# Performance work log

Measured on AMD Instinct MI355X. Metric: run time of the kernel, lower is better.

Reference implementation:

```python
import jax, jax.numpy as jnp
import numpy as np

NUM_HEADS = 8
HEAD_DIM = 64  # hidden_dim // num_heads = 512 // 8
THRESHOLD = 0.5


def setup_inputs() -> dict:
    key = jax.random.key(0)
    ks = jax.random.split(key, 12)
    B, T, D, Hd = 4, 1024, 512, 512
    s = 0.02
    inp = {
        'x': jax.random.normal(ks[0], (B, T, D), dtype=jnp.float32),
        'Wq': jax.random.normal(ks[1], (D, Hd), dtype=jnp.float32) * s,
        'bq': jnp.zeros((Hd,), jnp.float32),
        'Wk': jax.random.normal(ks[2], (D, Hd), dtype=jnp.float32) * s,
        'bk': jnp.zeros((Hd,), jnp.float32),
        'Wv': jax.random.normal(ks[3], (D, Hd), dtype=jnp.float32) * s,
        'bv': jnp.zeros((Hd,), jnp.float32),
        'conv_w': jax.random.normal(ks[4], (NUM_HEADS,), dtype=jnp.float32) * 0.3,
        'conv_b': jnp.zeros((1,), jnp.float32),
        'Wfh': jax.random.normal(ks[5], (Hd, Hd), dtype=jnp.float32) * s,
        'bfh': jnp.zeros((Hd,), jnp.float32),
        'Wfg': jax.random.normal(ks[6], (Hd, Hd), dtype=jnp.float32) * s,
        'bfg': jnp.zeros((Hd,), jnp.float32),
        'Wrh': jax.random.normal(ks[7], (Hd, Hd), dtype=jnp.float32) * s,
        'brh': jnp.zeros((Hd,), jnp.float32),
        'Wrg': jax.random.normal(ks[8], (Hd, Hd), dtype=jnp.float32) * s,
        'brg': jnp.zeros((Hd,), jnp.float32),
    }
    return inp


def reference(x, Wq, bq, Wk, bk, Wv, bv, conv_w, conv_b,
              Wfh, bfh, Wfg, bfg, Wrh, brh, Wrg, brg):
    B, T, D = x.shape
    H, hd = NUM_HEADS, HEAD_DIM
    scale = hd ** -0.5

    q = (x @ Wq + bq).reshape(B, T, H, hd).transpose(0, 2, 1, 3)  # [B,H,T,hd]
    k = (x @ Wk + bk).reshape(B, T, H, hd).transpose(0, 2, 1, 3)
    v = (x @ Wv + bv).reshape(B, T, H, hd).transpose(0, 2, 1, 3)

    scores = jnp.einsum('bhqd,bhkd->bhqk', q, k) * scale        # [B,H,T,T]
    A_t = jax.nn.softmax(scores, axis=-1)

    # cross-head 1x1 conv: weighted sum over heads -> [B,1,T,T]
    R_f = jax.nn.sigmoid(jnp.einsum('bhqk,h->bqk', A_t, conv_w) + conv_b[0])
    R_f = R_f[:, None]                                           # [B,1,T,T]
    M_f = (R_f <= THRESHOLD).astype(A_t.dtype)
    M_r = (1.0 - R_f <= THRESHOLD).astype(A_t.dtype)

    A_f = jax.nn.softmax(A_t * M_f, axis=-1)
    A_r = jax.nn.softmax(A_t * M_r, axis=-1)

    T_f = jnp.einsum('bhqk,bhkd->bhqd', A_f, v).transpose(0, 2, 1, 3).reshape(B, T, H * hd)
    T_r = jnp.einsum('bhqk,bhkd->bhqd', A_r, v).transpose(0, 2, 1, 3).reshape(B, T, H * hd)

    F_f = T_f @ Wfh + bfh
    G_f = jax.nn.sigmoid(T_f @ Wfg + bfg)
    F_r = T_r @ Wrh + brh
    G_r = jax.nn.sigmoid(T_r @ Wrg + brg)

    G_cat = jax.nn.softmax(jnp.stack([G_f, G_r], axis=-1), axis=-1)  # [B,T,Hd,2]
    F_t = F_f * G_cat[..., 0] + F_r * G_cat[..., 1]
    return F_t
```

## Files before the change

### kernel.cpp

```cpp
#include <hip/hip_runtime.h>
#include <hip/hip_bf16.h>
#include <stdint.h>

typedef short bf16x8 __attribute__((ext_vector_type(8)));
typedef float f32x4 __attribute__((ext_vector_type(4)));

__device__ __forceinline__ unsigned short f2bf(float f) {
  union { float f; unsigned int u; } v;
  v.f = f;
  unsigned int u = v.u;
  u = (u + 0x7fffu + ((u >> 16) & 1u)) >> 16;
  return (unsigned short)u;
}

__device__ __forceinline__ unsigned int cvt_pk_bf16(float lo, float hi) {
  unsigned int r;
  asm("v_cvt_pk_bf16_f32 %0, %1, %2" : "=v"(r) : "v"(lo), "v"(hi));
  return r;
}

typedef union { bf16x8 v; unsigned int u[4]; } frag_u;

__device__ __forceinline__ void gload16(const void* g, void* lds) {
  __builtin_amdgcn_global_load_lds(
      (const __attribute__((address_space(1))) unsigned int*)(unsigned long long)g,
      (__attribute__((address_space(3))) unsigned int*)(unsigned long long)(unsigned)(unsigned long long)lds,
      16, 0, 0);
}

__device__ __forceinline__ bf16x8 lds_frag(const unsigned short* t, int row, int ch4q) {
  return *(const bf16x8*)(t + row * 64 + ((ch4q ^ (row & 7)) << 3));
}


__global__ __launch_bounds__(256) void prep_kernel(
    const float* __restrict__ x,
    const float* __restrict__ Wq, const float* __restrict__ Wk, const float* __restrict__ Wv,
    const float* __restrict__ Wfh, const float* __restrict__ Wfg,
    const float* __restrict__ Wrh, const float* __restrict__ Wrg,
    unsigned short* __restrict__ xb, unsigned short* __restrict__ wt) {
  int bid = blockIdx.x;
  int tid = threadIdx.x;
  if (bid < 256) {
    const float4* xi = (const float4*)x;
#pragma unroll
    for (int rep = 0; rep < 8; rep++) {
      int i = bid * 256 + tid + rep * 65536;
      float4 v = xi[i];
      uint2 u;
      u.x = cvt_pk_bf16(v.x, v.y);
      u.y = cvt_pk_bf16(v.z, v.w);
      *(uint2*)&xb[(size_t)i * 4] = u;
    }
  } else {
    __shared__ float tile[64][65];
    int t = bid - 256;
    int mat = t >> 6;
    t &= 63;
    int tr = (t >> 3) * 64, tc = (t & 7) * 64;
    const float* W = (mat == 0) ? Wq : (mat == 1) ? Wk : (mat == 2) ? Wv
                   : (mat == 3) ? Wfh : (mat == 4) ? Wfg : (mat == 5) ? Wrh : Wrg;
    unsigned short* Wt = wt + (size_t)mat * 512 * 512;
    for (int rep = 0; rep < 16; rep++) {
      int idx = rep * 256 + tid;
      int r = idx >> 6, c = idx & 63;
      tile[r][c] = W[(tr + r) * 512 + tc + c];
    }
    __syncthreads();
    for (int rep = 0; rep < 16; rep++) {
      int idx = rep * 256 + tid;
      int r = idx >> 6, c = idx & 63;
      Wt[(tc + r) * 512 + tr + c] = f2bf(tile[c][r]);
    }
  }
}

__global__ __launch_bounds__(256, 3) void qkv_kernel(
    const unsigned short* __restrict__ xb,
    const unsigned short* __restrict__ wtq, const unsigned short* __restrict__ wtk,
    const unsigned short* __restrict__ wtv,
    const float* __restrict__ bq, const float* __restrict__ bk, const float* __restrict__ bv,
    unsigned short* __restrict__ Qfrag, unsigned short* __restrict__ Kfrag,
    unsigned short* __restrict__ Vfrag) {
  __shared__ __attribute__((aligned(16))) unsigned short smem[16384];
  unsigned short* As = smem;
  unsigned short* Bq = smem + 4096;
  unsigned short* Bk = smem + 8192;
  unsigned short* Bv = smem + 12288;
  unsigned short* st0 = smem;
  unsigned short* st1 = smem + 4608;
  unsigned short* st2 = smem + 9216;
  const int m0 = blockIdx.y * 64, n0 = blockIdx.x * 64;
  const int tid = threadIdx.x, w = tid >> 6, lane = tid & 63;
  const int c = lane & 15, quad = lane >> 4;
  const int wm = w & 1, wn = w >> 1;
  const int rsel = lane >> 3, csel = lane & 7;
  const int sc = csel ^ rsel;
  const char* Ag  = (const char*)xb  + (size_t)(m0 + w * 16 + rsel) * 1024 + sc * 16;
  const char* Bgq = (const char*)wtq + (size_t)(n0 + w * 16 + rsel) * 1024 + sc * 16;
  const char* Bgk = (const char*)wtk + (size_t)(n0 + w * 16 + rsel) * 1024 + sc * 16;
  const char* Bgv = (const char*)wtv + (size_t)(n0 + w * 16 + rsel) * 1024 + sc * 16;
  unsigned short* lA = &As[w * 1024];
  unsigned short* lQ = &Bq[w * 1024];
  unsigned short* lK = &Bk[w * 1024];
  unsigned short* lV = &Bv[w * 1024];

  f32x4 acc[3][2][2];
  f32x4 z4 = {0.f, 0.f, 0.f, 0.f};
#pragma unroll
  for (int o = 0; o < 3; o++)
#pragma unroll
    for (int i = 0; i < 2; i++)
#pragma unroll
      for (int j = 0; j < 2; j++) acc[o][i][j] = z4;

  for (int ks = 0; ks < 8; ks++) {
    if (ks) __syncthreads();
    const int kb = ks * 128;
    gload16(Ag + kb, lA);        gload16(Ag + kb + 8192, lA + 512);
    gload16(Bgq + kb, lQ);       gload16(Bgq + kb + 8192, lQ + 512);
    gload16(Bgk + kb, lK);       gload16(Bgk + kb + 8192, lK + 512);
    gload16(Bgv + kb, lV);       gload16(Bgv + kb + 8192, lV + 512);
    __syncthreads();
#pragma unroll
    for (int ch = 0; ch < 2; ch++) {
      const int cq = ch * 4 + quad;
      bf16x8 a0 = lds_frag(As, wm * 32 + c, cq);
      bf16x8 a1 = lds_frag(As, wm * 32 + 16 + c, cq);
#pragma unroll
      for (int nt = 0; nt < 2; nt++) {
        const int rb = wn * 32 + nt * 16 + c;
        bf16x8 fq = lds_frag(Bq, rb, cq);
        bf16x8 fk = lds_frag(Bk, rb, cq);
        bf16x8 fv = lds_frag(Bv, rb, cq);
        acc[0][0][nt] = __builtin_amdgcn_mfma_f32_16x16x32_bf16(a0, fq, acc[0][0][nt], 0, 0, 0);
        acc[0][1][nt] = __builtin_amdgcn_mfma_f32_16x16x32_bf16(a1, fq, acc[0][1][nt], 0, 0, 0);
        acc[1][0][nt] = __builtin_amdgcn_mfma_f32_16x16x32_bf16(a0, fk, acc[1][0][nt], 0, 0, 0);
        acc[1][1][nt] = __builtin_amdgcn_mfma_f32_16x16x32_bf16(a1, fk, acc[1][1][nt], 0, 0, 0);
        acc[2][0][nt] = __builtin_amdgcn_mfma_f32_16x16x32_bf16(a0, fv, acc[2][0][nt], 0, 0, 0);
        acc[2][1][nt] = __builtin_amdgcn_mfma_f32_16x16x32_bf16(a1, fv, acc[2][1][nt], 0, 0, 0);
      }
    }
  }
  __syncthreads();

#pragma unroll
  for (int ms = 0; ms < 2; ms++)
#pragma unroll
    for (int nt = 0; nt < 2; nt++) {
      int n_l = wn * 32 + nt * 16 + c;
      int n = n0 + n_l;
      float biasq = bq[n], biask = bk[n], biasv = bv[n];
#pragma unroll
      for (int r = 0; r < 4; r++) {
        int m_l = wm * 32 + ms * 16 + quad * 4 + r;
        st0[m_l * 72 + n_l] = f2bf((acc[0][ms][nt][r] + biasq) * 0.125f);
        st1[m_l * 72 + n_l] = f2bf(acc[1][ms][nt][r] + biask);
        st2[n_l * 72 + m_l] = f2bf(acc[2][ms][nt][r] + biasv);
      }
    }
  __syncthreads();

  {
    const int h = n0 >> 6;
    const int bb = m0 >> 10, t0b = (m0 & 1023) >> 4;
#pragma unroll
    for (int sub = 0; sub < 2; sub++) {
      uint4 vq = *(uint4*)&st0[(w * 16 + c) * 72 + sub * 32 + quad * 8];
      uint4 vk = *(uint4*)&st1[(w * 16 + c) * 72 + sub * 32 + quad * 8];
      size_t base = (size_t)((bb * 64 + t0b + w) * 8192) + h * 1024 + sub * 512 + lane * 8;
      *(uint4*)&Qfrag[base] = vq;
      *(uint4*)&Kfrag[base] = vk;
    }
    const int ktq = t0b + w;
    const int ktp = ktq >> 1, half = ktq & 1;
#pragma unroll
    for (int dm = 0; dm < 4; dm++) {
      uint2 vv = *(uint2*)&st2[(dm * 16 + c) * 72 + w * 16 + quad * 4];
      size_t base = (size_t)(bb * 8 + h) * 65536 + (size_t)(ktp * 4 + dm) * 512
                  + lane * 8 + half * 4;
      *(uint2*)&Vfrag[base] = vv;
    }
  }
}

__global__ __launch_bounds__(512, 4) void zgate_kernel(
    const unsigned short* __restrict__ Qfrag, const unsigned short* __restrict__ Kfrag,
    const float* __restrict__ conv_w, const float* __restrict__ conv_b,
    unsigned int* __restrict__ Mfrag, unsigned short* __restrict__ At) {
  const int b = blockIdx.x, qt = blockIdx.y;
  const int tid = threadIdx.x, w = tid >> 6, lane = tid & 63;
  const int c = lane & 15, quad = lane >> 4;
  __shared__ float zbuf[8][16];

  f32x4 z4 = {0.f, 0.f, 0.f, 0.f};
  const float cb = conv_b[0];
  const size_t qbase = (size_t)((b * 64 + qt) * 8192) + lane * 8;
  const int kt0 = w * 8;
  const size_t kb0 = (size_t)((b * 64 + kt0) * 8192) + lane * 8;
  unsigned short* atp = At + (size_t)(b * 64 + qt) * 8 * 32 * 512 + lane * 8;

  f32x4 g[8];
#pragma unroll
  for (int j = 0; j < 8; j++) g[j] = {cb, cb, cb, cb};

  for (int h = 0; h < 8; h++) {
    bf16x8 qf0 = *(const bf16x8*)&Qfrag[qbase + h * 1024];
    bf16x8 qf1 = *(const bf16x8*)&Qfrag[qbase + h * 1024 + 512];
    f32x4 p[8];
    float zh = 0.f;
#pragma unroll
    for (int j = 0; j < 8; j++) {
      const size_t kb = kb0 + (size_t)j * 8192 + h * 1024;
      bf16x8 kf0 = *(const bf16x8*)&Kfrag[kb];
      bf16x8 kf1 = *(const bf16x8*)&Kfrag[kb + 512];
      f32x4 s = __builtin_amdgcn_mfma_f32_16x16x32_bf16(kf0, qf0, z4, 0, 0, 0);
      s = __builtin_amdgcn_mfma_f32_16x16x32_bf16(kf1, qf1, s, 0, 0, 0);
      p[j][0] = __expf(s[0]); p[j][1] = __expf(s[1]);
      p[j][2] = __expf(s[2]); p[j][3] = __expf(s[3]);
      zh += (p[j][0] + p[j][1]) + (p[j][2] + p[j][3]);
    }
    zh += __shfl_xor(zh, 16); zh += __shfl_xor(zh, 32);
    __syncthreads();
    if (quad == 0) zbuf[w][c] = zh;
    __syncthreads();
    float Z = ((zbuf[0][c] + zbuf[1][c]) + (zbuf[2][c] + zbuf[3][c]))
            + ((zbuf[4][c] + zbuf[5][c]) + (zbuf[6][c] + zbuf[7][c]));
    const float izq = 1.0f / Z;
    const float cwz = conv_w[h] * izq;
    unsigned short* ath = atp + (size_t)h * 32 * 512;
#pragma unroll
    for (int j = 0; j < 4; j++) {
      uint4 u;
      u.x = cvt_pk_bf16(p[2 * j][0] * izq, p[2 * j][1] * izq);
      u.y = cvt_pk_bf16(p[2 * j][2] * izq, p[2 * j][3] * izq);
      u.z = cvt_pk_bf16(p[2 * j + 1][0] * izq, p[2 * j + 1][1] * izq);
      u.w = cvt_pk_bf16(p[2 * j + 1][2] * izq, p[2 * j + 1][3] * izq);
      *(uint4*)&ath[(size_t)(w * 4 + j) * 512] = u;
    }
#pragma unroll
    for (int j = 0; j < 8; j++) {
      g[j][0] += cwz * p[j][0]; g[j][1] += cwz * p[j][1];
      g[j][2] += cwz * p[j][2]; g[j][3] += cwz * p[j][3];
    }
  }

#pragma unroll
  for (int j = 0; j < 4; j++) {
    unsigned int p0 = 0, p1 = 0;
#pragma unroll
    for (int r = 0; r < 4; r++) {
      p0 |= ((g[2 * j][r] <= 0.f ? 1u : 0u) | (g[2 * j][r] >= 0.f ? 2u : 0u)) << (8 * r);
      p1 |= ((g[2 * j + 1][r] <= 0.f ? 1u : 0u) | (g[2 * j + 1][r] >= 0.f ? 2u : 0u)) << (8 * r);
    }
    const int ktp = w * 4 + j;
    uint2 mm; mm.x = p0; mm.y = p1;
    *(uint2*)&Mfrag[(size_t)(b * 64 + qt) * 4096 + (size_t)ktp * 128 + lane * 2] = mm;
  }
}

__global__ __launch_bounds__(256, 4) void pv_kernel(
    const unsigned short* __restrict__ At, const unsigned short* __restrict__ Vfrag,
    const unsigned int* __restrict__ Mfrag,
    unsigned short* __restrict__ Tfb, unsigned short* __restrict__ Trb) {
  const int h = blockIdx.x;
  const int b = blockIdx.y >> 5, qb = blockIdx.y & 31;
  const int tid = threadIdx.x, w = tid >> 6, lane = tid & 63;
  const int c = lane & 15, quad = lane >> 4;
  const int qloc = w & 1, kh = w >> 1;
  const int qt = qb * 2 + qloc;

  __shared__ __attribute__((aligned(16))) float red[2][4][256][4];
  __shared__ float zb[2][2][16];

  f32x4 z4 = {0.f, 0.f, 0.f, 0.f};
  const size_t abase = (size_t)((b * 64 + qt) * 8 + h) * 32 * 512 + lane * 8;
  const size_t mbase = (size_t)(b * 64 + qt) * 4096 + lane * 2;
  const size_t vb0 = (size_t)(b * 8 + h) * 65536 + lane * 8;

  frag_u ones;
  ones.u[0] = 0x3F803F80u; ones.u[1] = 0x3F803F80u;
  ones.u[2] = 0x3F803F80u; ones.u[3] = 0x3F803F80u;

  f32x4 accf[4], accr[4];
#pragma unroll
  for (int i = 0; i < 4; i++) { accf[i] = z4; accr[i] = z4; }
  f32x4 acc_zf = z4, acc_zr = z4;

#pragma unroll 2
  for (int ip = 0; ip < 16; ip++) {
    const int ktp = kh * 16 + ip;
    frag_u at;
    *(uint4*)&at.u[0] = *(const uint4*)&At[abase + (size_t)ktp * 512];
    const uint2 mp = *(const uint2*)&Mfrag[mbase + (size_t)ktp * 128];
    float e[8];
#pragma unroll
    for (int i = 0; i < 4; i++) {
      union { unsigned int u; float f; } lo, hi;
      lo.u = at.u[i] << 16;
      hi.u = at.u[i] & 0xffff0000u;
      e[2 * i]     = __expf(lo.f);
      e[2 * i + 1] = __expf(hi.f);
    }
    frag_u pF, pR;
    pF.u[0] = cvt_pk_bf16((mp.x & 0x1u)       ? e[0] : 1.f, (mp.x & 0x100u)     ? e[1] : 1.f);
    pF.u[1] = cvt_pk_bf16((mp.x & 0x10000u)   ? e[2] : 1.f, (mp.x & 0x1000000u) ? e[3] : 1.f);
    pF.u[2] = cvt_pk_bf16((mp.y & 0x1u)       ? e[4] : 1.f, (mp.y & 0x100u)     ? e[5] : 1.f);
    pF.u[3] = cvt_pk_bf16((mp.y & 0x10000u)   ? e[6] : 1.f, (mp.y & 0x1000000u) ? e[7] : 1.f);
    pR.u[0] = cvt_pk_bf16((mp.x & 0x2u)       ? e[0] : 1.f, (mp.x & 0x200u)     ? e[1] : 1.f);
    pR.u[1] = cvt_pk_bf16((mp.x & 0x20000u)   ? e[2] : 1.f, (mp.x & 0x2000000u) ? e[3] : 1.f);
    pR.u[2] = cvt_pk_bf16((mp.y & 0x2u)       ? e[4] : 1.f, (mp.y & 0x200u)     ? e[5] : 1.f);
    pR.u[3] = cvt_pk_bf16((mp.y & 0x20000u)   ? e[6] : 1.f, (mp.y & 0x2000000u) ? e[7] : 1.f);
    acc_zf = __builtin_amdgcn_mfma_f32_16x16x32_bf16(ones.v, pF.v, acc_zf, 0, 0, 0);
    acc_zr = __builtin_amdgcn_mfma_f32_16x16x32_bf16(ones.v, pR.v, acc_zr, 0, 0, 0);
#pragma unroll
    for (int dm = 0; dm < 4; dm++) {
      bf16x8 vf = *(const bf16x8*)&Vfrag[vb0 + (size_t)(ktp * 4 + dm) * 512];
      accf[dm] = __builtin_amdgcn_mfma_f32_16x16x32_bf16(vf, pF.v, accf[dm], 0, 0, 0);
      accr[dm] = __builtin_amdgcn_mfma_f32_16x16x32_bf16(vf, pR.v, accr[dm], 0, 0, 0);
    }
  }

  if (kh == 1) {
#pragma unroll
    for (int dm = 0; dm < 4; dm++) *(f32x4*)red[qloc][dm][lane] = accf[dm];
    if (lane < 16) { zb[qloc][0][lane] = acc_zf[0]; zb[qloc][1][lane] = acc_zr[0]; }
  }
  __syncthreads();
  if (kh == 0) {
#pragma unroll
    for (int dm = 0; dm < 4; dm++) accf[dm] += *(f32x4*)red[qloc][dm][lane];
  }
  __syncthreads();
  if (kh == 1) {
#pragma unroll
    for (int dm = 0; dm < 4; dm++) *(f32x4*)red[qloc][dm][lane] = accr[dm];
  }
  __syncthreads();
  uint2 outf[4], outr[4];
  if (kh == 0) {
#pragma unroll
    for (int dm = 0; dm < 4; dm++) accr[dm] += *(f32x4*)red[qloc][dm][lane];
    const float zf = acc_zf[0] + zb[qloc][0][c];
    const float zr = acc_zr[0] + zb[qloc][1][c];
    const float izf = 1.0f / zf, izr = 1.0f / zr;
#pragma unroll
    for (int dm = 0; dm < 4; dm++) {
      outf[dm].x = cvt_pk_bf16(accf[dm][0] * izf, accf[dm][1] * izf);
      outf[dm].y = cvt_pk_bf16(accf[dm][2] * izf, accf[dm][3] * izf);
      outr[dm].x = cvt_pk_bf16(accr[dm][0] * izr, accr[dm][1] * izr);
      outr[dm].y = cvt_pk_bf16(accr[dm][2] * izr, accr[dm][3] * izr);
    }
  }
  __syncthreads();
  unsigned short* ts = (unsigned short*)red;
  if (kh == 0) {
    const int qrow = qloc * 16 + c;
#pragma unroll
    for (int dm = 0; dm < 4; dm++) {
      *(uint2*)&ts[qrow * 72 + dm * 16 + quad * 4] = outf[dm];
      *(uint2*)&ts[(32 + qrow) * 72 + dm * 16 + quad * 4] = outr[dm];
    }
  }
  __syncthreads();
  {
    const int row = tid >> 3, seg = tid & 7;
    const size_t g = (size_t)(b * 1024 + qb * 32 + row) * 512 + h * 64 + seg * 8;
    *(uint4*)&Tfb[g] = *(uint4*)&ts[row * 72 + seg * 8];
    *(uint4*)&Trb[g] = *(uint4*)&ts[(32 + row) * 72 + seg * 8];
  }
}

__global__ __launch_bounds__(256, 4) void final_kernel(
    const unsigned short* __restrict__ Tfb, const unsigned short* __restrict__ Trb,
    const unsigned short* __restrict__ wfh, const unsigned short* __restrict__ wfg,
    const unsigned short* __restrict__ wrh, const unsigned short* __restrict__ wrg,
    const float* __restrict__ bfh, const float* __restrict__ bfg,
    const float* __restrict__ brh, const float* __restrict__ brg,
    float* __restrict__ out) {
  __shared__ unsigned short Atf[32 * 64];
  __shared__ unsigned short Atr[32 * 64];
  __shared__ unsigned short Bfh[64 * 64];
  __shared__ unsigned short Bfg[64 * 64];
  __shared__ unsigned short Brh[64 * 64];
  __shared__ unsigned short Brg[64 * 64];
  const int m0 = blockIdx.y * 32, n0 = blockIdx.x * 64;
  const int tid = threadIdx.x, w = tid >> 6, lane = tid & 63;
  const int c = lane & 15, quad = lane >> 4;
  const int wm = w & 1, wn = w >> 1;
  const int rsel = lane >> 3, csel = lane & 7;
  const int sc = csel ^ rsel;
  const char* Agf = (const char*)Tfb + (size_t)(m0 + w * 8 + rsel) * 1024 + sc * 16;
  const char* Agr = (const char*)Trb + (size_t)(m0 + w * 8 + rsel) * 1024 + sc * 16;
  const char* Bg0 = (const char*)wfh + (size_t)(n0 + w * 16 + rsel) * 1024 + sc * 16;
  const char* Bg1 = (const char*)wfg + (size_t)(n0 + w * 16 + rsel) * 1024 + sc * 16;
  const char* Bg2 = (const char*)wrh + (size_t)(n0 + w * 16 + rsel) * 1024 + sc * 16;
  const char* Bg3 = (const char*)wrg + (size_t)(n0 + w * 16 + rsel) * 1024 + sc * 16;
  unsigned short* lAf = &Atf[w * 512];
  unsigned short* lAr = &Atr[w * 512];
  unsigned short* l0 = &Bfh[w * 1024];
  unsigned short* l1 = &Bfg[w * 1024];
  unsigned short* l2 = &Brh[w * 1024];
  unsigned short* l3 = &Brg[w * 1024];

  f32x4 acc[4][2];
  f32x4 z4 = {0.f, 0.f, 0.f, 0.f};
#pragma unroll
  for (int o = 0; o < 4; o++)
#pragma unroll
    for (int j = 0; j < 2; j++) acc[o][j] = z4;

  for (int ks = 0; ks < 8; ks++) {
    if (ks) __syncthreads();
    const int kb = ks * 128;
    gload16(Agf + kb, lAf);
    gload16(Agr + kb, lAr);
    gload16(Bg0 + kb, l0);   gload16(Bg0 + kb + 8192, l0 + 512);
    gload16(Bg1 + kb, l1);   gload16(Bg1 + kb + 8192, l1 + 512);
    gload16(Bg2 + kb, l2);   gload16(Bg2 + kb + 8192, l2 + 512);
    gload16(Bg3 + kb, l3);   gload16(Bg3 + kb + 8192, l3 + 512);
    __syncthreads();
#pragma unroll
    for (int ch = 0; ch < 2; ch++) {
      const int cq = ch * 4 + quad;
      bf16x8 af = lds_frag(Atf, wm * 16 + c, cq);
      bf16x8 ar = lds_frag(Atr, wm * 16 + c, cq);
#pragma unroll
      for (int nt = 0; nt < 2; nt++) {
        const int rb = wn * 32 + nt * 16 + c;
        bf16x8 f0 = lds_frag(Bfh, rb, cq);
        bf16x8 f1 = lds_frag(Bfg, rb, cq);
        bf16x8 f2 = lds_frag(Brh, rb, cq);
        bf16x8 f3 = lds_frag(Brg, rb, cq);
        acc[0][nt] = __builtin_amdgcn_mfma_f32_16x16x32_bf16(af, f0, acc[0][nt], 0, 0, 0);
        acc[1][nt] = __builtin_amdgcn_mfma_f32_16x16x32_bf16(af, f1, acc[1][nt], 0, 0, 0);
        acc[2][nt] = __builtin_amdgcn_mfma_f32_16x16x32_bf16(ar, f2, acc[2][nt], 0, 0, 0);
        acc[3][nt] = __builtin_amdgcn_mfma_f32_16x16x32_bf16(ar, f3, acc[3][nt], 0, 0, 0);
      }
    }
  }

#pragma unroll
  for (int nt = 0; nt < 2; nt++) {
    int n = n0 + wn * 32 + nt * 16 + c;
    float b0 = bfh[n], b1 = bfg[n], b2 = brh[n], b3 = brg[n];
    int t0 = m0 + wm * 16 + quad * 4;
#pragma unroll
    for (int r = 0; r < 4; r++) {
      int t = t0 + r;
      float Ff = acc[0][nt][r] + b0;
      float Gf = 1.0f / (1.0f + __expf(-(acc[1][nt][r] + b1)));
      float Fr = acc[2][nt][r] + b2;
      float Gr = 1.0f / (1.0f + __expf(-(acc[3][nt][r] + b3)));
      float ef = __expf(Gf), er = __expf(Gr);
      out[(size_t)t * 512 + n] = (Ff * ef + Fr * er) / (ef + er);
    }
  }
}

extern "C" void kernel_launch(void* const* d_in, const int* in_sizes, int n_in,
                              void* d_out, int out_size, void* d_ws, size_t ws_size,
                              hipStream_t stream) {
  const float* x   = (const float*)d_in[0];
  const float* Wq  = (const float*)d_in[1];
  const float* bq  = (const float*)d_in[2];
  const float* Wk  = (const float*)d_in[3];
  const float* bk  = (const float*)d_in[4];
  const float* Wv  = (const float*)d_in[5];
  const float* bv  = (const float*)d_in[6];
  const float* cw  = (const float*)d_in[7];
  const float* cb  = (const float*)d_in[8];
  const float* Wfh = (const float*)d_in[9];
  const float* bfh = (const float*)d_in[10];
  const float* Wfg = (const float*)d_in[11];
  const float* bfg = (const float*)d_in[12];
  const float* Wrh = (const float*)d_in[13];
  const float* brh = (const float*)d_in[14];
  const float* Wrg = (const float*)d_in[15];
  const float* brg = (const float*)d_in[16];

  char* ws = (char*)d_ws;
  const size_t MB = 1024 * 1024;
  unsigned short* xb    = (unsigned short*)(ws + 0 * MB);
  unsigned short* Qfrag = (unsigned short*)(ws + 4 * MB);
  unsigned short* Kfrag = (unsigned short*)(ws + 8 * MB);
  unsigned short* Vfrag = (unsigned short*)(ws + 12 * MB);
  unsigned short* Tfb   = (unsigned short*)(ws + 16 * MB);
  unsigned short* Trb   = (unsigned short*)(ws + 20 * MB);
  unsigned short* wt    = (unsigned short*)(ws + 24 * MB);
  unsigned int*   Mfrag = (unsigned int*)(ws + 28 * MB);
  unsigned short* At    = (unsigned short*)(ws + 36 * MB);
  const size_t WSZ = 512 * 512;

  prep_kernel<<<704, 256, 0, stream>>>(x, Wq, Wk, Wv, Wfh, Wfg, Wrh, Wrg, xb, wt);
  qkv_kernel<<<dim3(8, 64), 256, 0, stream>>>(xb, wt + 0 * WSZ, wt + 1 * WSZ, wt + 2 * WSZ,
                                              bq, bk, bv, Qfrag, Kfrag, Vfrag);
  zgate_kernel<<<dim3(4, 64), 512, 0, stream>>>(Qfrag, Kfrag, cw, cb, Mfrag, At);
  pv_kernel<<<dim3(8, 128), 256, 0, stream>>>(At, Vfrag, Mfrag, Tfb, Trb);
  final_kernel<<<dim3(8, 128), 256, 0, stream>>>(Tfb, Trb, wt + 3 * WSZ, wt + 4 * WSZ,
                                                 wt + 5 * WSZ, wt + 6 * WSZ,
                                                 bfh, bfg, brh, brg, (float*)d_out);
}
```

Baseline: 179.6 us.

## Fuse gate and PV kernels by recomputing QK scores instead of storing attention

```diff
diff --git a/kernel.cpp b/kernel.cpp
--- a/kernel.cpp
+++ b/kernel.cpp
@@ -184,26 +184,30 @@
   }
 }
 
-__global__ __launch_bounds__(512, 4) void zgate_kernel(
+__global__ __launch_bounds__(512, 4) void attn_kernel(
     const unsigned short* __restrict__ Qfrag, const unsigned short* __restrict__ Kfrag,
+    const unsigned short* __restrict__ Vfrag,
     const float* __restrict__ conv_w, const float* __restrict__ conv_b,
-    unsigned int* __restrict__ Mfrag, unsigned short* __restrict__ At) {
+    unsigned short* __restrict__ Tfb, unsigned short* __restrict__ Trb) {
   const int b = blockIdx.x, qt = blockIdx.y;
   const int tid = threadIdx.x, w = tid >> 6, lane = tid & 63;
   const int c = lane & 15, quad = lane >> 4;
   __shared__ float zbuf[8][16];
+  __shared__ __attribute__((aligned(16))) float red[2 * 8 * 4 * 64 * 4];
+  __shared__ float zred[2][8][16];
 
   f32x4 z4 = {0.f, 0.f, 0.f, 0.f};
   const float cb = conv_b[0];
   const size_t qbase = (size_t)((b * 64 + qt) * 8192) + lane * 8;
-  const int kt0 = w * 8;
-  const size_t kb0 = (size_t)((b * 64 + kt0) * 8192) + lane * 8;
-  unsigned short* atp = At + (size_t)(b * 64 + qt) * 8 * 32 * 512 + lane * 8;
-
+  const size_t kb0 = (size_t)((b * 64 + w * 8) * 8192) + lane * 8;
+  const size_t vb0 = (size_t)(b * 8) * 65536 + lane * 8;
+
+  float izq[8];
   f32x4 g[8];
 #pragma unroll
   for (int j = 0; j < 8; j++) g[j] = {cb, cb, cb, cb};
 
+#pragma unroll
   for (int h = 0; h < 8; h++) {
     bf16x8 qf0 = *(const bf16x8*)&Qfrag[qbase + h * 1024];
     bf16x8 qf1 = *(const bf16x8*)&Qfrag[qbase + h * 1024 + 512];
@@ -226,18 +230,8 @@
     __syncthreads();
     float Z = ((zbuf[0][c] + zbuf[1][c]) + (zbuf[2][c] + zbuf[3][c]))
             + ((zbuf[4][c] + zbuf[5][c]) + (zbuf[6][c] + zbuf[7][c]));
-    const float izq = 1.0f / Z;
-    const float cwz = conv_w[h] * izq;
-    unsigned short* ath = atp + (size_t)h * 32 * 512;
-#pragma unroll
-    for (int j = 0; j < 4; j++) {
-      uint4 u;
-      u.x = cvt_pk_bf16(p[2 * j][0] * izq, p[2 * j][1] * izq);
-      u.y = cvt_pk_bf16(p[2 * j][2] * izq, p[2 * j][3] * izq);
-      u.z = cvt_pk_bf16(p[2 * j + 1][0] * izq, p[2 * j + 1][1] * izq);
-      u.w = cvt_pk_bf16(p[2 * j + 1][2] * izq, p[2 * j + 1][3] * izq);
-      *(uint4*)&ath[(size_t)(w * 4 + j) * 512] = u;
-    }
+    izq[h] = 1.0f / Z;
+    const float cwz = conv_w[h] * izq[h];
 #pragma unroll
     for (int j = 0; j < 8; j++) {
       g[j][0] += cwz * p[j][0]; g[j][1] += cwz * p[j][1];
@@ -245,129 +239,92 @@
     }
   }
 
-#pragma unroll
-  for (int j = 0; j < 4; j++) {
+  unsigned int mmx[4], mmy[4];
+#pragma unroll
+  for (int t = 0; t < 4; t++) {
     unsigned int p0 = 0, p1 = 0;
 #pragma unroll
     for (int r = 0; r < 4; r++) {
-      p0 |= ((g[2 * j][r] <= 0.f ? 1u : 0u) | (g[2 * j][r] >= 0.f ? 2u : 0u)) << (8 * r);
-      p1 |= ((g[2 * j + 1][r] <= 0.f ? 1u : 0u) | (g[2 * j + 1][r] >= 0.f ? 2u : 0u)) << (8 * r);
-    }
-    const int ktp = w * 4 + j;
-    uint2 mm; mm.x = p0; mm.y = p1;
-    *(uint2*)&Mfrag[(size_t)(b * 64 + qt) * 4096 + (size_t)ktp * 128 + lane * 2] = mm;
-  }
-}
-
-__global__ __launch_bounds__(256, 4) void pv_kernel(
-    const unsigned short* __restrict__ At, const unsigned short* __restrict__ Vfrag,
-    const unsigned int* __restrict__ Mfrag,
-    unsigned short* __restrict__ Tfb, unsigned short* __restrict__ Trb) {
-  const int h = blockIdx.x;
-  const int b = blockIdx.y >> 5, qb = blockIdx.y & 31;
-  const int tid = threadIdx.x, w = tid >> 6, lane = tid & 63;
-  const int c = lane & 15, quad = lane >> 4;
-  const int qloc = w & 1, kh = w >> 1;
-  const int qt = qb * 2 + qloc;
-
-  __shared__ __attribute__((aligned(16))) float red[2][4][256][4];
-  __shared__ float zb[2][2][16];
-
-  f32x4 z4 = {0.f, 0.f, 0.f, 0.f};
-  const size_t abase = (size_t)((b * 64 + qt) * 8 + h) * 32 * 512 + lane * 8;
-  const size_t mbase = (size_t)(b * 64 + qt) * 4096 + lane * 2;
-  const size_t vb0 = (size_t)(b * 8 + h) * 65536 + lane * 8;
+      p0 |= ((g[2 * t][r] <= 0.f ? 1u : 0u) | (g[2 * t][r] >= 0.f ? 2u : 0u)) << (8 * r);
+      p1 |= ((g[2 * t + 1][r] <= 0.f ? 1u : 0u) | (g[2 * t + 1][r] >= 0.f ? 2u : 0u)) << (8 * r);
+    }
+    mmx[t] = p0; mmy[t] = p1;
+  }
 
   frag_u ones;
   ones.u[0] = 0x3F803F80u; ones.u[1] = 0x3F803F80u;
   ones.u[2] = 0x3F803F80u; ones.u[3] = 0x3F803F80u;
 
-  f32x4 accf[4], accr[4];
-#pragma unroll
-  for (int i = 0; i < 4; i++) { accf[i] = z4; accr[i] = z4; }
-  f32x4 acc_zf = z4, acc_zr = z4;
-
-#pragma unroll 2
-  for (int ip = 0; ip < 16; ip++) {
-    const int ktp = kh * 16 + ip;
-    frag_u at;
-    *(uint4*)&at.u[0] = *(const uint4*)&At[abase + (size_t)ktp * 512];
-    const uint2 mp = *(const uint2*)&Mfrag[mbase + (size_t)ktp * 128];
-    float e[8];
-#pragma unroll
-    for (int i = 0; i < 4; i++) {
-      union { unsigned int u; float f; } lo, hi;
-      lo.u = at.u[i] << 16;
-      hi.u = at.u[i] & 0xffff0000u;
-      e[2 * i]     = __expf(lo.f);
-      e[2 * i + 1] = __expf(hi.f);
-    }
-    frag_u pF, pR;
-    pF.u[0] = cvt_pk_bf16((mp.x & 0x1u)       ? e[0] : 1.f, (mp.x & 0x100u)     ? e[1] : 1.f);
-    pF.u[1] = cvt_pk_bf16((mp.x & 0x10000u)   ? e[2] : 1.f, (mp.x & 0x1000000u) ? e[3] : 1.f);
-    pF.u[2] = cvt_pk_bf16((mp.y & 0x1u)       ? e[4] : 1.f, (mp.y & 0x100u)     ? e[5] : 1.f);
-    pF.u[3] = cvt_pk_bf16((mp.y & 0x10000u)   ? e[6] : 1.f, (mp.y & 0x1000000u) ? e[7] : 1.f);
-    pR.u[0] = cvt_pk_bf16((mp.x & 0x2u)       ? e[0] : 1.f, (mp.x & 0x200u)     ? e[1] : 1.f);
-    pR.u[1] = cvt_pk_bf16((mp.x & 0x20000u)   ? e[2] : 1.f, (mp.x & 0x2000000u) ? e[3] : 1.f);
-    pR.u[2] = cvt_pk_bf16((mp.y & 0x2u)       ? e[4] : 1.f, (mp.y & 0x200u)     ? e[5] : 1.f);
-    pR.u[3] = cvt_pk_bf16((mp.y & 0x20000u)   ? e[6] : 1.f, (mp.y & 0x2000000u) ? e[7] : 1.f);
-    acc_zf = __builtin_amdgcn_mfma_f32_16x16x32_bf16(ones.v, pF.v, acc_zf, 0, 0, 0);
-    acc_zr = __builtin_amdgcn_mfma_f32_16x16x32_bf16(ones.v, pR.v, acc_zr, 0, 0, 0);
+  const int fr = w >> 2, dmslot = w & 3;
+  const size_t tbase = (size_t)(b * 1024 + qt * 16 + c) * 512;
+  unsigned short* dstsel = (fr == 0) ? Tfb : Trb;
+
+#pragma unroll
+  for (int h = 0; h < 8; h++) {
+    bf16x8 qf0 = *(const bf16x8*)&Qfrag[qbase + h * 1024];
+    bf16x8 qf1 = *(const bf16x8*)&Qfrag[qbase + h * 1024 + 512];
+    const float iz_h = izq[h];
+    f32x4 accf[4], accr[4];
+#pragma unroll
+    for (int i = 0; i < 4; i++) { accf[i] = z4; accr[i] = z4; }
+    f32x4 zf4 = z4, zr4 = z4;
+#pragma unroll
+    for (int t = 0; t < 4; t++) {
+      const size_t kba = kb0 + (size_t)(2 * t) * 8192 + h * 1024;
+      const size_t kbb = kba + 8192;
+      bf16x8 ka0 = *(const bf16x8*)&Kfrag[kba];
+      bf16x8 ka1 = *(const bf16x8*)&Kfrag[kba + 512];
+      bf16x8 kb0f = *(const bf16x8*)&Kfrag[kbb];
+      bf16x8 kb1f = *(const bf16x8*)&Kfrag[kbb + 512];
+      f32x4 sa = __builtin_amdgcn_mfma_f32_16x16x32_bf16(ka0, qf0, z4, 0, 0, 0);
+      sa = __builtin_amdgcn_mfma_f32_16x16x32_bf16(ka1, qf1, sa, 0, 0, 0);
+      f32x4 sb = __builtin_amdgcn_mfma_f32_16x16x32_bf16(kb0f, qf0, z4, 0, 0, 0);
+      sb = __builtin_amdgcn_mfma_f32_16x16x32_bf16(kb1f, qf1, sb, 0, 0, 0);
+      float ea[4], eb[4];
+#pragma unroll
+      for (int r = 0; r < 4; r++) {
+        ea[r] = __expf(__expf(sa[r]) * iz_h);
+        eb[r] = __expf(__expf(sb[r]) * iz_h);
+      }
+      frag_u pF, pR;
+      pF.u[0] = cvt_pk_bf16((mmx[t] & 0x1u)       ? ea[0] : 1.f, (mmx[t] & 0x100u)     ? ea[1] : 1.f);
+      pF.u[1] = cvt_pk_bf16((mmx[t] & 0x10000u)   ? ea[2] : 1.f, (mmx[t] & 0x1000000u) ? ea[3] : 1.f);
+      pF.u[2] = cvt_pk_bf16((mmy[t] & 0x1u)       ? eb[0] : 1.f, (mmy[t] & 0x100u)     ? eb[1] : 1.f);
+      pF.u[3] = cvt_pk_bf16((mmy[t] & 0x10000u)   ? eb[2] : 1.f, (mmy[t] & 0x1000000u) ? eb[3] : 1.f);
+      pR.u[0] = cvt_pk_bf16((mmx[t] & 0x2u)       ? ea[0] : 1.f, (mmx[t] & 0x200u)     ? ea[1] : 1.f);
+      pR.u[1] = cvt_pk_bf16((mmx[t] & 0x20000u)   ? ea[2] : 1.f, (mmx[t] & 0x2000000u) ? ea[3] : 1.f);
+      pR.u[2] = cvt_pk_bf16((mmy[t] & 0x2u)       ? eb[0] : 1.f, (mmy[t] & 0x200u)     ? eb[1] : 1.f);
+      pR.u[3] = cvt_pk_bf16((mmy[t] & 0x20000u)   ? eb[2] : 1.f, (mmy[t] & 0x2000000u) ? eb[3] : 1.f);
+      zf4 = __builtin_amdgcn_mfma_f32_16x16x32_bf16(ones.v, pF.v, zf4, 0, 0, 0);
+      zr4 = __builtin_amdgcn_mfma_f32_16x16x32_bf16(ones.v, pR.v, zr4, 0, 0, 0);
+      const size_t vbh = vb0 + (size_t)h * 65536 + (size_t)((w * 4 + t) * 4) * 512;
+#pragma unroll
+      for (int dm = 0; dm < 4; dm++) {
+        bf16x8 vf = *(const bf16x8*)&Vfrag[vbh + (size_t)dm * 512];
+        accf[dm] = __builtin_amdgcn_mfma_f32_16x16x32_bf16(vf, pF.v, accf[dm], 0, 0, 0);
+        accr[dm] = __builtin_amdgcn_mfma_f32_16x16x32_bf16(vf, pR.v, accr[dm], 0, 0, 0);
+      }
+    }
+    __syncthreads();
 #pragma unroll
     for (int dm = 0; dm < 4; dm++) {
-      bf16x8 vf = *(const bf16x8*)&Vfrag[vb0 + (size_t)(ktp * 4 + dm) * 512];
-      accf[dm] = __builtin_amdgcn_mfma_f32_16x16x32_bf16(vf, pF.v, accf[dm], 0, 0, 0);
-      accr[dm] = __builtin_amdgcn_mfma_f32_16x16x32_bf16(vf, pR.v, accr[dm], 0, 0, 0);
-    }
-  }
-
-  if (kh == 1) {
-#pragma unroll
-    for (int dm = 0; dm < 4; dm++) *(f32x4*)red[qloc][dm][lane] = accf[dm];
-    if (lane < 16) { zb[qloc][0][lane] = acc_zf[0]; zb[qloc][1][lane] = acc_zr[0]; }
-  }
-  __syncthreads();
-  if (kh == 0) {
-#pragma unroll
-    for (int dm = 0; dm < 4; dm++) accf[dm] += *(f32x4*)red[qloc][dm][lane];
-  }
-  __syncthreads();
-  if (kh == 1) {
-#pragma unroll
-    for (int dm = 0; dm < 4; dm++) *(f32x4*)red[qloc][dm][lane] = accr[dm];
-  }
-  __syncthreads();
-  uint2 outf[4], outr[4];
-  if (kh == 0) {
-#pragma unroll
-    for (int dm = 0; dm < 4; dm++) accr[dm] += *(f32x4*)red[qloc][dm][lane];
-    const float zf = acc_zf[0] + zb[qloc][0][c];
-    const float zr = acc_zr[0] + zb[qloc][1][c];
-    const float izf = 1.0f / zf, izr = 1.0f / zr;
-#pragma unroll
-    for (int dm = 0; dm < 4; dm++) {
-      outf[dm].x = cvt_pk_bf16(accf[dm][0] * izf, accf[dm][1] * izf);
-      outf[dm].y = cvt_pk_bf16(accf[dm][2] * izf, accf[dm][3] * izf);
-      outr[dm].x = cvt_pk_bf16(accr[dm][0] * izr, accr[dm][1] * izr);
-      outr[dm].y = cvt_pk_bf16(accr[dm][2] * izr, accr[dm][3] * izr);
-    }
-  }
-  __syncthreads();
-  unsigned short* ts = (unsigned short*)red;
-  if (kh == 0) {
-    const int qrow = qloc * 16 + c;
-#pragma unroll
-    for (int dm = 0; dm < 4; dm++) {
-      *(uint2*)&ts[qrow * 72 + dm * 16 + quad * 4] = outf[dm];
-      *(uint2*)&ts[(32 + qrow) * 72 + dm * 16 + quad * 4] = outr[dm];
-    }
-  }
-  __syncthreads();
-  {
-    const int row = tid >> 3, seg = tid & 7;
-    const size_t g = (size_t)(b * 1024 + qb * 32 + row) * 512 + h * 64 + seg * 8;
-    *(uint4*)&Tfb[g] = *(uint4*)&ts[row * 72 + seg * 8];
-    *(uint4*)&Trb[g] = *(uint4*)&ts[(32 + row) * 72 + seg * 8];
+      *(f32x4*)&red[(((0 * 8 + w) * 4 + dm) * 64 + lane) * 4] = accf[dm];
+      *(f32x4*)&red[(((1 * 8 + w) * 4 + dm) * 64 + lane) * 4] = accr[dm];
+    }
+    if (quad == 0) { zred[0][w][c] = zf4[0]; zred[1][w][c] = zr4[0]; }
+    __syncthreads();
+    f32x4 o = z4;
+#pragma unroll
+    for (int w2 = 0; w2 < 8; w2++)
+      o += *(const f32x4*)&red[(((fr * 8 + w2) * 4 + dmslot) * 64 + lane) * 4];
+    float Zq = 0.f;
+#pragma unroll
+    for (int w2 = 0; w2 < 8; w2++) Zq += zred[fr][w2][c];
+    const float iz = 1.0f / Zq;
+    uint2 u;
+    u.x = cvt_pk_bf16(o[0] * iz, o[1] * iz);
+    u.y = cvt_pk_bf16(o[2] * iz, o[3] * iz);
+    *(uint2*)&dstsel[tbase + h * 64 + dmslot * 16 + quad * 4] = u;
   }
 }
 
@@ -488,15 +445,12 @@
   unsigned short* Tfb   = (unsigned short*)(ws + 16 * MB);
   unsigned short* Trb   = (unsigned short*)(ws + 20 * MB);
   unsigned short* wt    = (unsigned short*)(ws + 24 * MB);
-  unsigned int*   Mfrag = (unsigned int*)(ws + 28 * MB);
-  unsigned short* At    = (unsigned short*)(ws + 36 * MB);
   const size_t WSZ = 512 * 512;
 
   prep_kernel<<<704, 256, 0, stream>>>(x, Wq, Wk, Wv, Wfh, Wfg, Wrh, Wrg, xb, wt);
   qkv_kernel<<<dim3(8, 64), 256, 0, stream>>>(xb, wt + 0 * WSZ, wt + 1 * WSZ, wt + 2 * WSZ,
                                               bq, bk, bv, Qfrag, Kfrag, Vfrag);
-  zgate_kernel<<<dim3(4, 64), 512, 0, stream>>>(Qfrag, Kfrag, cw, cb, Mfrag, At);
-  pv_kernel<<<dim3(8, 128), 256, 0, stream>>>(At, Vfrag, Mfrag, Tfb, Trb);
+  attn_kernel<<<dim3(4, 64), 512, 0, stream>>>(Qfrag, Kfrag, Vfrag, cw, cb, Tfb, Trb);
   final_kernel<<<dim3(8, 128), 256, 0, stream>>>(Tfb, Trb, wt + 3 * WSZ, wt + 4 * WSZ,
                                                  wt + 5 * WSZ, wt + 6 * WSZ,
                                                  bfh, bfg, brh, brg, (float*)d_out);
```

Result: slower. 263.0 us (+46.5%).
